# Performance work log

Hardware: AMD Instinct MI355X
Metric: run time of the kernel (lower is better)

Reference implementation:

```python
import jax, jax.numpy as jnp
import numpy as np

VOCAB, EMB, SEQ_TOK, NHID, NLAYERS, NTOKEN = 400000, 300, 25, 256, 2, 2


def _lstm_layer(x, h0, c0, W_ih, W_hh, b_ih, b_hh):
    # x: [T, B, in], PyTorch gate order i, f, g, o
    def step(carry, xt):
        h, c = carry
        gates = xt @ W_ih.T + h @ W_hh.T + (b_ih + b_hh)
        i, f, g, o = jnp.split(gates, 4, axis=-1)
        c = jax.nn.sigmoid(f) * c + jax.nn.sigmoid(i) * jnp.tanh(g)
        h = jax.nn.sigmoid(o) * jnp.tanh(c)
        return (h, c), h
    (hT, cT), ys = jax.lax.scan(step, (h0, c0), x)
    return ys, hT, cT


def setup_inputs() -> dict:
    key = jax.random.key(0)
    ks = jax.random.split(key, 16)
    s = 0.05
    inp = {
        "input": jax.random.randint(ks[0], (1024, SEQ_TOK), 0, VOCAB),
        "h0": jnp.zeros((NLAYERS, 1024, NHID), jnp.float32),
        "c0": jnp.zeros((NLAYERS, 1024, NHID), jnp.float32),
        "emb_table": jax.random.normal(ks[1], (VOCAB, EMB), jnp.float32) * s,
        "fc_w": jax.random.normal(ks[2], (10, NHID), jnp.float32) * s,
        "fc_b": jnp.zeros((10,), jnp.float32),
        "dec_w": jax.random.normal(ks[3], (NTOKEN, 10), jnp.float32) * s,
        "dec_b": jnp.zeros((NTOKEN,), jnp.float32),
    }
    in_dims = [SEQ_TOK, NHID]
    for l in range(NLAYERS):
        inp[f"W_ih{l}"] = jax.random.normal(ks[4 + 4 * l], (4 * NHID, in_dims[l]), jnp.float32) * s
        inp[f"W_hh{l}"] = jax.random.normal(ks[5 + 4 * l], (4 * NHID, NHID), jnp.float32) * s
        inp[f"b_ih{l}"] = jnp.zeros((4 * NHID,), jnp.float32)
        inp[f"b_hh{l}"] = jnp.zeros((4 * NHID,), jnp.float32)
    return inp


def reference(input, h0, c0, emb_table, fc_w, fc_b, dec_w, dec_b,
              W_ih0, W_hh0, b_ih0, b_hh0, W_ih1, W_hh1, b_ih1, b_hh1):
    tokens = input.T                      # [25, B]
    B = tokens.shape[1]
    emb = emb_table[tokens]               # vectorized gather: [25, B, 300]
    emb = emb.reshape(300, B, 25)         # faithful to torch .view(300, B, 25)
    x = emb
    Ws = [(W_ih0, W_hh0, b_ih0, b_hh0), (W_ih1, W_hh1, b_ih1, b_hh1)]
    hs, cs = [], []
    for l in range(NLAYERS):
        x, hT, cT = _lstm_layer(x, h0[l], c0[l], *Ws[l])
        hs.append(hT); cs.append(cT)
    output = x                            # [300, B, nhid]
    hidden = (jnp.stack(hs), jnp.stack(cs))
    fc_out = jax.nn.relu(output @ fc_w.T + fc_b)  # [300, B, 10]
    decoded = fc_out[-1] @ dec_w.T + dec_b        # [B, ntoken]
    return (decoded.T, hidden[0], hidden[1])      # decoded.t(), (h, c)
```

## Files before the change

kernel.cpp:

```cpp
#include <hip/hip_runtime.h>
#include <stdint.h>

#define TSTEPS 300
#define BATCH  1024
#define MB     16
#define NWG    (BATCH / MB)
#define FRAGS_L0 36
#define FRAGS_L1 64
#define FRAGS_PW (FRAGS_L0 + FRAGS_L1)

typedef __bf16 bf16x8 __attribute__((ext_vector_type(8)));
typedef float  f32x4  __attribute__((ext_vector_type(4)));

__device__ __forceinline__ uint16_t f2bf(float f) {
  uint32_t u = __builtin_bit_cast(uint32_t, f);
  u += 0x7fffu + ((u >> 16) & 1u);
  return (uint16_t)(u >> 16);
}
__device__ __forceinline__ float bf2f(uint16_t h) {
  uint32_t u = ((uint32_t)h) << 16;
  return __builtin_bit_cast(float, u);
}
__device__ __forceinline__ float sigm(float x) { return 1.0f / (1.0f + __expf(-x)); }
__device__ __forceinline__ float tanh_(float x) {
  float e = __expf(2.0f * x);
  return (e - 1.0f) / (e + 1.0f);
}

__global__ void gather_x(const int* __restrict__ tok, const float* __restrict__ emb,
                         uint16_t* __restrict__ Xf) {
  int idx = blockIdx.x * 256 + threadIdx.x;
  int t    = idx >> 15;
  int rem  = idx & 32767;
  int wg   = rem >> 9;
  int e512 = rem & 511;
  int lane = e512 >> 3;
  int jj   = e512 & 7;
  int m = lane & 15, quad = lane >> 4;
  int k = quad * 8 + jj;
  float v = 0.0f;
  if (k < 25) {
    int b = wg * 16 + m;
    int n = (t * 1024 + b) * 25 + k;
    int s  = n / 307200;
    int r2 = n - s * 307200;
    int bb = r2 / 300;
    int e  = r2 - bb * 300;
    int token = tok[bb * 25 + s];
    v = emb[(size_t)token * 300 + e];
  }
  Xf[idx] = f2bf(v);
}

__global__ void pack_w(const float* __restrict__ Wih0, const float* __restrict__ Whh0,
                       const float* __restrict__ Wih1, const float* __restrict__ Whh1,
                       uint16_t* __restrict__ Wp) {
  int idx = blockIdx.x * 256 + threadIdx.x;
  int w   = idx / 51200;
  int rem = idx - w * 51200;
  int frag = rem >> 9;
  int e    = rem & 511;
  int lane = e >> 3, jj = e & 7;
  int nl = lane & 15, quad = lane >> 4;
  int kk = quad * 8 + jj;
  float v;
  if (frag < FRAGS_L0) {
    int ks = frag >> 2, nt = frag & 3;
    int n = nt * 256 + w * 16 + nl;
    if (ks == 0) v = (kk < 25) ? Wih0[n * 25 + kk] : 0.0f;
    else         v = Whh0[n * 256 + (ks - 1) * 32 + kk];
  } else {
    int f1 = frag - FRAGS_L0;
    int ks = f1 >> 2, nt = f1 & 3;
    int n = nt * 256 + w * 16 + nl;
    int k = ks * 32 + kk;
    v = (k < 256) ? Wih1[n * 256 + k] : Whh1[n * 256 + (k - 256)];
  }
  Wp[idx] = f2bf(v);
}

__global__ __launch_bounds__(1024, 4) void lstm_main(
    const float* __restrict__ h0in, const float* __restrict__ c0in,
    const float* __restrict__ fcw,  const float* __restrict__ fcb,
    const float* __restrict__ decw, const float* __restrict__ decb,
    const float* __restrict__ bih0, const float* __restrict__ bhh0,
    const float* __restrict__ bih1, const float* __restrict__ bhh1,
    const uint16_t* __restrict__ Xf, const uint16_t* __restrict__ Wp,
    float* __restrict__ out) {
  __shared__ uint16_t h0s[2][16][264];
  __shared__ uint16_t h1s[2][16][264];
  __shared__ float fcs[16][10];

  const int wg   = blockIdx.x;
  const int tid  = threadIdx.x;
  const int w    = tid >> 6;
  const int lane = tid & 63;
  const int jl   = lane & 15;
  const int quad = lane >> 4;
  const int jcol = w * 16 + jl;

  for (int idx = tid; idx < 16 * 256; idx += 1024) {
    int r = idx >> 8, k = idx & 255;
    int b = wg * 16 + r;
    h0s[0][r][k] = f2bf(h0in[(size_t)b * 256 + k]);
    h1s[0][r][k] = f2bf(h0in[262144 + (size_t)b * 256 + k]);
  }
  float c0r[4], c1r[4], h0v[4], h1v[4];
#pragma unroll
  for (int r = 0; r < 4; r++) {
    size_t b = wg * 16 + quad * 4 + r;
    c0r[r] = c0in[b * 256 + jcol];
    c1r[r] = c0in[262144 + b * 256 + jcol];
  }
  float bias0[4], bias1[4];
#pragma unroll
  for (int nt = 0; nt < 4; nt++) {
    int n = nt * 256 + jcol;
    bias0[nt] = bih0[n] + bhh0[n];
    bias1[nt] = bih1[n] + bhh1[n];
  }
  __syncthreads();

  const uint4* pw = (const uint4*)Wp + (size_t)(w * FRAGS_PW) * 64 + lane;
  const uint4* px = (const uint4*)Xf;

  int p = 0;
  for (int t = 0; t < TSTEPS; t++) {
    f32x4 acc[4];
#pragma unroll
    for (int nt = 0; nt < 4; nt++)
      acc[nt] = (f32x4){bias0[nt], bias0[nt], bias0[nt], bias0[nt]};
    {
      bf16x8 afrag = __builtin_bit_cast(bf16x8, px[((size_t)t * 64 + wg) * 64 + lane]);
      bf16x8 bfrag[4];
#pragma unroll
      for (int nt = 0; nt < 4; nt++)
        bfrag[nt] = __builtin_bit_cast(bf16x8, pw[nt * 64]);
#pragma unroll
      for (int ks = 0; ks <= 8; ks++) {
        bf16x8 anext = afrag;
        bf16x8 bnext[4] = {bfrag[0], bfrag[1], bfrag[2], bfrag[3]};
        if (ks < 8) {
          anext = __builtin_bit_cast(bf16x8,
                    *(const uint4*)&h0s[p][jl][ks * 32 + quad * 8]);
#pragma unroll
          for (int nt = 0; nt < 4; nt++)
            bnext[nt] = __builtin_bit_cast(bf16x8, pw[((ks + 1) * 4 + nt) * 64]);
        }
#pragma unroll
        for (int nt = 0; nt < 4; nt++)
          acc[nt] = __builtin_amdgcn_mfma_f32_16x16x32_bf16(afrag, bfrag[nt], acc[nt], 0, 0, 0);
        afrag = anext;
#pragma unroll
        for (int nt = 0; nt < 4; nt++) bfrag[nt] = bnext[nt];
      }
    }
#pragma unroll
    for (int r = 0; r < 4; r++) {
      float gi = sigm(acc[0][r]);
      float gf = sigm(acc[1][r]);
      float gg = tanh_(acc[2][r]);
      float go = sigm(acc[3][r]);
      float c = gf * c0r[r] + gi * gg;
      c0r[r] = c;
      float h = go * tanh_(c);
      h0v[r] = h;
      h0s[1 - p][quad * 4 + r][jcol] = f2bf(h);
    }
    __syncthreads();

#pragma unroll
    for (int nt = 0; nt < 4; nt++)
      acc[nt] = (f32x4){bias1[nt], bias1[nt], bias1[nt], bias1[nt]};
    {
      bf16x8 afrag = __builtin_bit_cast(bf16x8,
                       *(const uint4*)&h0s[1 - p][jl][quad * 8]);
      bf16x8 bfrag[4];
#pragma unroll
      for (int nt = 0; nt < 4; nt++)
        bfrag[nt] = __builtin_bit_cast(bf16x8, pw[(FRAGS_L0 + nt) * 64]);
#pragma unroll
      for (int ks = 0; ks < 16; ks++) {
        bf16x8 anext = afrag;
        bf16x8 bnext[4] = {bfrag[0], bfrag[1], bfrag[2], bfrag[3]};
        if (ks < 15) {
          int ksn = ks + 1;
          const uint16_t* abase = (ksn < 8)
              ? &h0s[1 - p][jl][ksn * 32 + quad * 8]
              : &h1s[p][jl][(ksn - 8) * 32 + quad * 8];
          anext = __builtin_bit_cast(bf16x8, *(const uint4*)abase);
#pragma unroll
          for (int nt = 0; nt < 4; nt++)
            bnext[nt] = __builtin_bit_cast(bf16x8, pw[(FRAGS_L0 + ksn * 4 + nt) * 64]);
        }
#pragma unroll
        for (int nt = 0; nt < 4; nt++)
          acc[nt] = __builtin_amdgcn_mfma_f32_16x16x32_bf16(afrag, bfrag[nt], acc[nt], 0, 0, 0);
        afrag = anext;
#pragma unroll
        for (int nt = 0; nt < 4; nt++) bfrag[nt] = bnext[nt];
      }
    }
#pragma unroll
    for (int r = 0; r < 4; r++) {
      float gi = sigm(acc[0][r]);
      float gf = sigm(acc[1][r]);
      float gg = tanh_(acc[2][r]);
      float go = sigm(acc[3][r]);
      float c = gf * c1r[r] + gi * gg;
      c1r[r] = c;
      float h = go * tanh_(c);
      h1v[r] = h;
      h1s[1 - p][quad * 4 + r][jcol] = f2bf(h);
    }
    __syncthreads();
    p ^= 1;
  }

  float* outH = out + 2048;
  float* outC = out + 2048 + 524288;
#pragma unroll
  for (int r = 0; r < 4; r++) {
    size_t b = wg * 16 + quad * 4 + r;
    outH[b * 256 + jcol]          = h0v[r];
    outH[262144 + b * 256 + jcol] = h1v[r];
    outC[b * 256 + jcol]          = c0r[r];
    outC[262144 + b * 256 + jcol] = c1r[r];
  }
  if (tid < 160) {
    int r = tid / 10, ju = tid - r * 10;
    float s = fcb[ju];
    for (int k = 0; k < 256; k++)
      s += bf2f(h1s[p][r][k]) * fcw[ju * 256 + k];
    fcs[r][ju] = fmaxf(s, 0.0f);
  }
  __syncthreads();
  if (tid < 32) {
    int r = tid & 15, m = tid >> 4;
    float d = decb[m];
#pragma unroll
    for (int q = 0; q < 10; q++) d += fcs[r][q] * decw[m * 10 + q];
    out[(size_t)m * 1024 + wg * 16 + r] = d;
  }
}

extern "C" void kernel_launch(void* const* d_in, const int* in_sizes, int n_in,
                              void* d_out, int out_size, void* d_ws, size_t ws_size,
                              hipStream_t stream) {
  const int*   tok  = (const int*)d_in[0];
  const float* h0   = (const float*)d_in[1];
  const float* c0   = (const float*)d_in[2];
  const float* emb  = (const float*)d_in[3];
  const float* fcw  = (const float*)d_in[4];
  const float* fcb  = (const float*)d_in[5];
  const float* decw = (const float*)d_in[6];
  const float* decb = (const float*)d_in[7];
  const float* Wih0 = (const float*)d_in[8];
  const float* Whh0 = (const float*)d_in[9];
  const float* bih0 = (const float*)d_in[10];
  const float* bhh0 = (const float*)d_in[11];
  const float* Wih1 = (const float*)d_in[12];
  const float* Whh1 = (const float*)d_in[13];
  const float* bih1 = (const float*)d_in[14];
  const float* bhh1 = (const float*)d_in[15];

  uint16_t* Xf  = (uint16_t*)d_ws;
  uint16_t* Wpk = Xf + 9830400;

  gather_x<<<38400, 256, 0, stream>>>(tok, emb, Xf);
  pack_w<<<3200, 256, 0, stream>>>(Wih0, Whh0, Wih1, Whh1, Wpk);
  lstm_main<<<NWG, 1024, 0, stream>>>(h0, c0, fcw, fcb, decw, decb,
                                      bih0, bhh0, bih1, bhh1, Xf, Wpk,
                                      (float*)d_out);
}
```

Baseline: 13.33 ms.

## Split hidden units across four cooperative blocks per batch group with register-resident weights

Each 16-row batch group is now served by four workgroups instead of one. Each workgroup owns a quarter of the hidden units and keeps its slice of the packed weights in registers for the whole run, so weights are no longer reloaded from global memory every timestep. The kernel launches cooperatively with 256 blocks, and each step the blocks exchange their hidden-state slices through global memory with release/acquire flags and spin-waits. This raises the number of active CUs and removes the per-step weight traffic. The cost is cross-block synchronisation latency on the critical path every step, plus heavy register pressure from holding 50 fragments per lane.

```diff
diff --git a/kernel.cpp b/kernel.cpp
--- a/kernel.cpp
+++ b/kernel.cpp
@@ -2,12 +2,11 @@
 #include <stdint.h>
 
 #define TSTEPS 300
-#define BATCH  1024
-#define MB     16
-#define NWG    (BATCH / MB)
-#define FRAGS_L0 36
-#define FRAGS_L1 64
-#define FRAGS_PW (FRAGS_L0 + FRAGS_L1)
+#define NGROUP 64
+#define NSPLIT 4
+#define NBLK   (NGROUP * NSPLIT)
+#define NW     8
+#define FRAGS  50
 
 typedef __bf16 bf16x8 __attribute__((ext_vector_type(8)));
 typedef float  f32x4  __attribute__((ext_vector_type(4)));
@@ -56,191 +55,249 @@
                        const float* __restrict__ Wih1, const float* __restrict__ Whh1,
                        uint16_t* __restrict__ Wp) {
   int idx = blockIdx.x * 256 + threadIdx.x;
-  int w   = idx / 51200;
-  int rem = idx - w * 51200;
-  int frag = rem >> 9;
-  int e    = rem & 511;
+  int e  = idx & 511;
+  int fg = idx >> 9;
+  int f  = fg % FRAGS;
+  int wv = (fg / FRAGS) & 7;
+  int s  = fg / (FRAGS * 8);
   int lane = e >> 3, jj = e & 7;
-  int nl = lane & 15, quad = lane >> 4;
-  int kk = quad * 8 + jj;
+  int nl = lane & 15, kk = (lane >> 4) * 8 + jj;
+  int ks, tl;
+  bool l1 = (f >= 18);
+  if (!l1) { ks = f >> 1; tl = f & 1; }
+  else     { int f1 = f - 18; ks = f1 >> 1; tl = f1 & 1; }
+  int n = (wv >> 1) * 256 + s * 64 + (wv & 1) * 32 + tl * 16 + nl;
   float v;
-  if (frag < FRAGS_L0) {
-    int ks = frag >> 2, nt = frag & 3;
-    int n = nt * 256 + w * 16 + nl;
+  if (!l1) {
     if (ks == 0) v = (kk < 25) ? Wih0[n * 25 + kk] : 0.0f;
     else         v = Whh0[n * 256 + (ks - 1) * 32 + kk];
   } else {
-    int f1 = frag - FRAGS_L0;
-    int ks = f1 >> 2, nt = f1 & 3;
-    int n = nt * 256 + w * 16 + nl;
     int k = ks * 32 + kk;
     v = (k < 256) ? Wih1[n * 256 + k] : Whh1[n * 256 + (k - 256)];
   }
   Wp[idx] = f2bf(v);
 }
 
-__global__ __launch_bounds__(1024, 4) void lstm_main(
+__global__ __launch_bounds__(512, 2) void lstm_main(
     const float* __restrict__ h0in, const float* __restrict__ c0in,
     const float* __restrict__ fcw,  const float* __restrict__ fcb,
     const float* __restrict__ decw, const float* __restrict__ decb,
     const float* __restrict__ bih0, const float* __restrict__ bhh0,
     const float* __restrict__ bih1, const float* __restrict__ bhh1,
     const uint16_t* __restrict__ Xf, const uint16_t* __restrict__ Wp,
-    float* __restrict__ out) {
-  __shared__ uint16_t h0s[2][16][264];
-  __shared__ uint16_t h1s[2][16][264];
-  __shared__ float fcs[16][10];
-
-  const int wg   = blockIdx.x;
+    uint16_t* __restrict__ xh0, uint16_t* __restrict__ xh1,
+    int* __restrict__ flags, float* __restrict__ out)
+{
+  __shared__ uint16_t h0s[16][264];
+  __shared__ uint16_t h1s[16][264];
+  __shared__ float    gl[16][260];
+  __shared__ float    fcs[16][10];
+
+  const int bid  = blockIdx.x;
+  const int s    = bid >> 6;
+  const int g    = bid & 63;
   const int tid  = threadIdx.x;
   const int w    = tid >> 6;
   const int lane = tid & 63;
   const int jl   = lane & 15;
   const int quad = lane >> 4;
-  const int jcol = w * 16 + jl;
-
-  for (int idx = tid; idx < 16 * 256; idx += 1024) {
+
+  const uint4* pw = (const uint4*)Wp + ((size_t)(s * NW + w) * FRAGS) * 64 + lane;
+  bf16x8 wr[FRAGS];
+#pragma unroll
+  for (int i = 0; i < FRAGS; i++)
+    wr[i] = __builtin_bit_cast(bf16x8, pw[i * 64]);
+
+  const int ncol = (w >> 1) * 256 + s * 64 + (w & 1) * 32 + jl;
+  const float bA0 = bih0[ncol]      + bhh0[ncol];
+  const float bA1 = bih0[ncol + 16] + bhh0[ncol + 16];
+  const float bB0 = bih1[ncol]      + bhh1[ncol];
+  const float bB1 = bih1[ncol + 16] + bhh1[ncol + 16];
+
+  for (int idx = tid; idx < 16 * 256; idx += 512) {
     int r = idx >> 8, k = idx & 255;
-    int b = wg * 16 + r;
-    h0s[0][r][k] = f2bf(h0in[(size_t)b * 256 + k]);
-    h1s[0][r][k] = f2bf(h0in[262144 + (size_t)b * 256 + k]);
-  }
-  float c0r[4], c1r[4], h0v[4], h1v[4];
-#pragma unroll
-  for (int r = 0; r < 4; r++) {
-    size_t b = wg * 16 + quad * 4 + r;
-    c0r[r] = c0in[b * 256 + jcol];
-    c1r[r] = c0in[262144 + b * 256 + jcol];
-  }
-  float bias0[4], bias1[4];
-#pragma unroll
-  for (int nt = 0; nt < 4; nt++) {
-    int n = nt * 256 + jcol;
-    bias0[nt] = bih0[n] + bhh0[n];
-    bias1[nt] = bih1[n] + bhh1[n];
-  }
+    size_t b = (size_t)g * 16 + r;
+    h0s[r][k] = f2bf(h0in[b * 256 + k]);
+    h1s[r][k] = f2bf(h0in[262144 + b * 256 + k]);
+  }
+
+  const int ur = tid >> 6;
+  const int uh = tid & 63;
+  const size_t cb = ((size_t)g * 16 + ur) * 256 + s * 64 + uh;
+  float c0_a = c0in[cb],           c0_b = c0in[cb + 8 * 256];
+  float c1_a = c0in[262144 + cb],  c1_b = c0in[262144 + cb + 8 * 256];
+  float h0_a = 0.f, h0_b = 0.f, h1_a = 0.f, h1_b = 0.f;
+
+  const int ci = tid & 127;
+  const int cs = tid >> 7;
+  const int sp = (s + 1 + cs) & 3;
+  const int cr = ci >> 3;
+  const int cc = (ci & 7) * 8;
+
   __syncthreads();
 
-  const uint4* pw = (const uint4*)Wp + (size_t)(w * FRAGS_PW) * 64 + lane;
   const uint4* px = (const uint4*)Xf;
-
-  int p = 0;
+  uint4 xf = px[((size_t)0 * 64 + g) * 64 + lane];
+
+  const int gcb = (w >> 1) * 64 + (w & 1) * 32 + jl;
+
+#pragma unroll 1
   for (int t = 0; t < TSTEPS; t++) {
-    f32x4 acc[4];
-#pragma unroll
-    for (int nt = 0; nt < 4; nt++)
-      acc[nt] = (f32x4){bias0[nt], bias0[nt], bias0[nt], bias0[nt]};
-    {
-      bf16x8 afrag = __builtin_bit_cast(bf16x8, px[((size_t)t * 64 + wg) * 64 + lane]);
-      bf16x8 bfrag[4];
-#pragma unroll
-      for (int nt = 0; nt < 4; nt++)
-        bfrag[nt] = __builtin_bit_cast(bf16x8, pw[nt * 64]);
+    const size_t xpar = ((size_t)((t & 1) * 64 + g) * 4);
+
+    f32x4 acc0 = {bA0, bA0, bA0, bA0};
+    f32x4 acc1 = {bA1, bA1, bA1, bA1};
+    {
+      bf16x8 a = __builtin_bit_cast(bf16x8, xf);
 #pragma unroll
       for (int ks = 0; ks <= 8; ks++) {
-        bf16x8 anext = afrag;
-        bf16x8 bnext[4] = {bfrag[0], bfrag[1], bfrag[2], bfrag[3]};
-        if (ks < 8) {
-          anext = __builtin_bit_cast(bf16x8,
-                    *(const uint4*)&h0s[p][jl][ks * 32 + quad * 8]);
-#pragma unroll
-          for (int nt = 0; nt < 4; nt++)
-            bnext[nt] = __builtin_bit_cast(bf16x8, pw[((ks + 1) * 4 + nt) * 64]);
-        }
-#pragma unroll
-        for (int nt = 0; nt < 4; nt++)
-          acc[nt] = __builtin_amdgcn_mfma_f32_16x16x32_bf16(afrag, bfrag[nt], acc[nt], 0, 0, 0);
-        afrag = anext;
-#pragma unroll
-        for (int nt = 0; nt < 4; nt++) bfrag[nt] = bnext[nt];
+        bf16x8 an;
+        if (ks < 8) an = *(const bf16x8*)&h0s[jl][ks * 32 + quad * 8];
+        acc0 = __builtin_amdgcn_mfma_f32_16x16x32_bf16(a, wr[2 * ks],     acc0, 0, 0, 0);
+        acc1 = __builtin_amdgcn_mfma_f32_16x16x32_bf16(a, wr[2 * ks + 1], acc1, 0, 0, 0);
+        a = an;
       }
     }
 #pragma unroll
     for (int r = 0; r < 4; r++) {
-      float gi = sigm(acc[0][r]);
-      float gf = sigm(acc[1][r]);
-      float gg = tanh_(acc[2][r]);
-      float go = sigm(acc[3][r]);
-      float c = gf * c0r[r] + gi * gg;
-      c0r[r] = c;
-      float h = go * tanh_(c);
-      h0v[r] = h;
-      h0s[1 - p][quad * 4 + r][jcol] = f2bf(h);
-    }
-    __syncthreads();
-
-#pragma unroll
-    for (int nt = 0; nt < 4; nt++)
-      acc[nt] = (f32x4){bias1[nt], bias1[nt], bias1[nt], bias1[nt]};
-    {
-      bf16x8 afrag = __builtin_bit_cast(bf16x8,
-                       *(const uint4*)&h0s[1 - p][jl][quad * 8]);
-      bf16x8 bfrag[4];
-#pragma unroll
-      for (int nt = 0; nt < 4; nt++)
-        bfrag[nt] = __builtin_bit_cast(bf16x8, pw[(FRAGS_L0 + nt) * 64]);
+      gl[quad * 4 + r][gcb]      = acc0[r];
+      gl[quad * 4 + r][gcb + 16] = acc1[r];
+    }
+    __syncthreads();
+
+    {
+      float i1 = sigm (gl[ur][uh]);
+      float f1 = sigm (gl[ur][64 + uh]);
+      float g1 = tanh_(gl[ur][128 + uh]);
+      float o1 = sigm (gl[ur][192 + uh]);
+      c0_a = f1 * c0_a + i1 * g1;
+      h0_a = o1 * tanh_(c0_a);
+      float i2 = sigm (gl[ur + 8][uh]);
+      float f2 = sigm (gl[ur + 8][64 + uh]);
+      float g2 = tanh_(gl[ur + 8][128 + uh]);
+      float o2 = sigm (gl[ur + 8][192 + uh]);
+      c0_b = f2 * c0_b + i2 * g2;
+      h0_b = o2 * tanh_(c0_b);
+      uint16_t ha = f2bf(h0_a), hb = f2bf(h0_b);
+      h0s[ur][s * 64 + uh]     = ha;
+      h0s[ur + 8][s * 64 + uh] = hb;
+      size_t xb = (xpar + s) * 1024;
+      xh0[xb + ur * 64 + uh]       = ha;
+      xh0[xb + (ur + 8) * 64 + uh] = hb;
+    }
+    __threadfence();
+    __syncthreads();
+
+    if (tid == 0)
+      __hip_atomic_store(&flags[s * 64 + g], t + 1,
+                         __ATOMIC_RELEASE, __HIP_MEMORY_SCOPE_AGENT);
+    if (cs < 3) {
+      int* fp = &flags[sp * 64 + g];
+      while (__hip_atomic_load(fp, __ATOMIC_ACQUIRE, __HIP_MEMORY_SCOPE_AGENT) < t + 1)
+        __builtin_amdgcn_s_sleep(1);
+      const uint4* src = (const uint4*)xh0 + (xpar + sp) * 128;
+      uint4 v = src[ci];
+      *(uint4*)&h0s[cr][sp * 64 + cc] = v;
+    }
+    __syncthreads();
+
+    {
+      int tn = (t < TSTEPS - 1) ? t + 1 : t;
+      xf = px[((size_t)tn * 64 + g) * 64 + lane];
+    }
+    acc0 = (f32x4){bB0, bB0, bB0, bB0};
+    acc1 = (f32x4){bB1, bB1, bB1, bB1};
+    {
+      bf16x8 a = *(const bf16x8*)&h0s[jl][quad * 8];
 #pragma unroll
       for (int ks = 0; ks < 16; ks++) {
-        bf16x8 anext = afrag;
-        bf16x8 bnext[4] = {bfrag[0], bfrag[1], bfrag[2], bfrag[3]};
+        bf16x8 an;
         if (ks < 15) {
           int ksn = ks + 1;
-          const uint16_t* abase = (ksn < 8)
-              ? &h0s[1 - p][jl][ksn * 32 + quad * 8]
-              : &h1s[p][jl][(ksn - 8) * 32 + quad * 8];
-          anext = __builtin_bit_cast(bf16x8, *(const uint4*)abase);
-#pragma unroll
-          for (int nt = 0; nt < 4; nt++)
-            bnext[nt] = __builtin_bit_cast(bf16x8, pw[(FRAGS_L0 + ksn * 4 + nt) * 64]);
+          const uint16_t* ab = (ksn < 8) ? &h0s[jl][ksn * 32 + quad * 8]
+                                         : &h1s[jl][(ksn - 8) * 32 + quad * 8];
+          an = *(const bf16x8*)ab;
         }
-#pragma unroll
-        for (int nt = 0; nt < 4; nt++)
-          acc[nt] = __builtin_amdgcn_mfma_f32_16x16x32_bf16(afrag, bfrag[nt], acc[nt], 0, 0, 0);
-        afrag = anext;
-#pragma unroll
-        for (int nt = 0; nt < 4; nt++) bfrag[nt] = bnext[nt];
+        acc0 = __builtin_amdgcn_mfma_f32_16x16x32_bf16(a, wr[18 + 2 * ks],     acc0, 0, 0, 0);
+        acc1 = __builtin_amdgcn_mfma_f32_16x16x32_bf16(a, wr[18 + 2 * ks + 1], acc1, 0, 0, 0);
+        a = an;
       }
     }
 #pragma unroll
     for (int r = 0; r < 4; r++) {
-      float gi = sigm(acc[0][r]);
-      float gf = sigm(acc[1][r]);
-      float gg = tanh_(acc[2][r]);
-      float go = sigm(acc[3][r]);
-      float c = gf * c1r[r] + gi * gg;
-      c1r[r] = c;
-      float h = go * tanh_(c);
-      h1v[r] = h;
-      h1s[1 - p][quad * 4 + r][jcol] = f2bf(h);
-    }
-    __syncthreads();
-    p ^= 1;
+      gl[quad * 4 + r][gcb]      = acc0[r];
+      gl[quad * 4 + r][gcb + 16] = acc1[r];
+    }
+    __syncthreads();
+
+    {
+      float i1 = sigm (gl[ur][uh]);
+      float f1 = sigm (gl[ur][64 + uh]);
+      float g1 = tanh_(gl[ur][128 + uh]);
+      float o1 = sigm (gl[ur][192 + uh]);
+      c1_a = f1 * c1_a + i1 * g1;
+      h1_a = o1 * tanh_(c1_a);
+      float i2 = sigm (gl[ur + 8][uh]);
+      float f2 = sigm (gl[ur + 8][64 + uh]);
+      float g2 = tanh_(gl[ur + 8][128 + uh]);
+      float o2 = sigm (gl[ur + 8][192 + uh]);
+      c1_b = f2 * c1_b + i2 * g2;
+      h1_b = o2 * tanh_(c1_b);
+      uint16_t ha = f2bf(h1_a), hb = f2bf(h1_b);
+      h1s[ur][s * 64 + uh]     = ha;
+      h1s[ur + 8][s * 64 + uh] = hb;
+      size_t xb = (xpar + s) * 1024;
+      xh1[xb + ur * 64 + uh]       = ha;
+      xh1[xb + (ur + 8) * 64 + uh] = hb;
+    }
+    __threadfence();
+    __syncthreads();
+
+    if (tid == 0)
+      __hip_atomic_store(&flags[256 + s * 64 + g], t + 1,
+                         __ATOMIC_RELEASE, __HIP_MEMORY_SCOPE_AGENT);
+    if (cs < 3) {
+      int* fp = &flags[256 + sp * 64 + g];
+      while (__hip_atomic_load(fp, __ATOMIC_ACQUIRE, __HIP_MEMORY_SCOPE_AGENT) < t + 1)
+        __builtin_amdgcn_s_sleep(1);
+      const uint4* src = (const uint4*)xh1 + (xpar + sp) * 128;
+      uint4 v = src[ci];
+      *(uint4*)&h1s[cr][sp * 64 + cc] = v;
+    }
+    __syncthreads();
   }
 
   float* outH = out + 2048;
   float* outC = out + 2048 + 524288;
-#pragma unroll
-  for (int r = 0; r < 4; r++) {
-    size_t b = wg * 16 + quad * 4 + r;
-    outH[b * 256 + jcol]          = h0v[r];
-    outH[262144 + b * 256 + jcol] = h1v[r];
-    outC[b * 256 + jcol]          = c0r[r];
-    outC[262144 + b * 256 + jcol] = c1r[r];
-  }
-  if (tid < 160) {
-    int r = tid / 10, ju = tid - r * 10;
-    float s = fcb[ju];
-    for (int k = 0; k < 256; k++)
-      s += bf2f(h1s[p][r][k]) * fcw[ju * 256 + k];
-    fcs[r][ju] = fmaxf(s, 0.0f);
-  }
-  __syncthreads();
-  if (tid < 32) {
-    int r = tid & 15, m = tid >> 4;
-    float d = decb[m];
-#pragma unroll
-    for (int q = 0; q < 10; q++) d += fcs[r][q] * decw[m * 10 + q];
-    out[(size_t)m * 1024 + wg * 16 + r] = d;
+  {
+    size_t ba = (size_t)g * 16 + ur;
+    size_t oa = ba * 256 + s * 64 + uh;
+    outH[oa]           = h0_a;
+    outH[262144 + oa]  = h1_a;
+    outC[oa]           = c0_a;
+    outC[262144 + oa]  = c1_a;
+    size_t ob = oa + 8 * 256;
+    outH[ob]           = h0_b;
+    outH[262144 + ob]  = h1_b;
+    outC[ob]           = c0_b;
+    outC[262144 + ob]  = c1_b;
+  }
+  if (s == 0) {
+    if (tid < 160) {
+      int r = tid / 10, j = tid - r * 10;
+      float acc = fcb[j];
+      for (int k = 0; k < 256; k++)
+        acc += bf2f(h1s[r][k]) * fcw[j * 256 + k];
+      fcs[r][j] = fmaxf(acc, 0.0f);
+    }
+    __syncthreads();
+    if (tid < 32) {
+      int r = tid & 15, m = tid >> 4;
+      float d = decb[m];
+#pragma unroll
+      for (int q = 0; q < 10; q++) d += fcs[r][q] * decw[m * 10 + q];
+      out[(size_t)m * 1024 + g * 16 + r] = d;
+    }
   }
 }
 
@@ -264,12 +321,23 @@
   const float* bih1 = (const float*)d_in[14];
   const float* bhh1 = (const float*)d_in[15];
 
-  uint16_t* Xf  = (uint16_t*)d_ws;
-  uint16_t* Wpk = Xf + 9830400;
-
+  uint16_t* Xf   = (uint16_t*)d_ws;
+  uint16_t* Wpk  = Xf  + 9830400;
+  uint16_t* xh0  = Wpk + 819200;
+  uint16_t* xh1  = xh0 + 524288;
+  int*      flg  = (int*)(xh1 + 524288);
+
+  hipMemsetAsync(flg, 0, 512 * sizeof(int), stream);
   gather_x<<<38400, 256, 0, stream>>>(tok, emb, Xf);
   pack_w<<<3200, 256, 0, stream>>>(Wih0, Whh0, Wih1, Whh1, Wpk);
-  lstm_main<<<NWG, 1024, 0, stream>>>(h0, c0, fcw, fcb, decw, decb,
-                                      bih0, bhh0, bih1, bhh1, Xf, Wpk,
-                                      (float*)d_out);
-}
+
+  float* outp = (float*)d_out;
+  void* args[16] = {
+    (void*)&h0,  (void*)&c0,  (void*)&fcw,  (void*)&fcb,
+    (void*)&decw,(void*)&decb,(void*)&bih0, (void*)&bhh0,
+    (void*)&bih1,(void*)&bhh1,(void*)&Xf,   (void*)&Wpk,
+    (void*)&xh0, (void*)&xh1, (void*)&flg,  (void*)&outp
+  };
+  hipLaunchCooperativeKernel((const void*)lstm_main, dim3(NBLK), dim3(512),
+                             args, 0, stream);
+}
```

Result: slower. 32.15 ms (+141.1%).
